# Kernel tuning notes

Hardware: AMD Instinct MI355X
Metric: run time of the kernel (lower is better)

The kernel has to match this reference:

```python
import jax, jax.numpy as jnp
import numpy as np

D_MODEL = 1024
NUM_HEADS = 16
D_K = D_MODEL // NUM_HEADS


def setup_inputs() -> dict:
    key = jax.random.key(0)
    k1, k2, k3, k4 = jax.random.split(key, 4)
    scale = 1.0 / np.sqrt(D_MODEL)
    inp = {
        "input": jax.random.normal(k1, (2, 2048, D_MODEL), dtype=jnp.float32),
        "W_qkv": jax.random.normal(k2, (D_MODEL, 3 * D_MODEL), dtype=jnp.float32) * scale,
        "b_qkv": jax.random.normal(k3, (3 * D_MODEL,), dtype=jnp.float32) * 0.02,
        "W_out": jax.random.normal(k4, (D_MODEL, D_MODEL), dtype=jnp.float32) * scale,
    }
    return inp


def reference(input, W_qkv, b_qkv, W_out):
    B, S, _ = input.shape
    qkv = input @ W_qkv + b_qkv                      # [B,S,3D]
    q, k, v = jnp.split(qkv, 3, axis=-1)             # each [B,S,D]
    def heads(x):
        return x.reshape(B, S, NUM_HEADS, D_K).transpose(0, 2, 1, 3)  # [B,H,S,dk]
    q, k, v = heads(q), heads(k), heads(v)
    scores = jnp.einsum("bhsd,bhtd->bhst", q, k) / jnp.sqrt(jnp.float32(D_K))
    attn = jax.nn.softmax(scores, axis=-1)           # [B,H,S,S]
    out = jnp.einsum("bhst,bhtd->bhsd", attn, v)     # [B,H,S,dk]
    out = out.transpose(0, 2, 1, 3).reshape(B, S, D_MODEL)
    return out @ W_out
```

## Files before the change

### kernel.cpp

```cpp
#include <hip/hip_runtime.h>

typedef unsigned short u16;
typedef unsigned int u32;
typedef __attribute__((ext_vector_type(8))) short short8;
typedef __attribute__((ext_vector_type(8))) __bf16 bf16x8;
typedef __attribute__((ext_vector_type(4))) float f32x4;
typedef __attribute__((ext_vector_type(16))) float f32x16;

__device__ __forceinline__ u16 f2bf(float f) {
  union { float f; u32 u; } c; c.f = f;
  u32 u = c.u + 0x7fffu + ((c.u >> 16) & 1u);
  return (u16)(u >> 16);
}
__device__ __forceinline__ f32x4 mfma16(short8 a, short8 b, f32x4 c) {
  return __builtin_amdgcn_mfma_f32_16x16x32_bf16(
      __builtin_bit_cast(bf16x8, a), __builtin_bit_cast(bf16x8, b), c, 0, 0, 0);
}
__device__ __forceinline__ f32x16 mfma32(short8 a, short8 b, f32x16 c) {
  return __builtin_amdgcn_mfma_f32_32x32x16_bf16(
      __builtin_bit_cast(bf16x8, a), __builtin_bit_cast(bf16x8, b), c, 0, 0, 0);
}
__device__ __forceinline__ float fexp2(float x) {
  float r; asm("v_exp_f32 %0, %1" : "=v"(r) : "v"(x)); return r;
}
__device__ __forceinline__ void gl16(const u16* g, u16* l) {
  __builtin_amdgcn_global_load_lds(
      (const __attribute__((address_space(1))) unsigned*)g,
      (__attribute__((address_space(3))) unsigned*)l, 16, 0, 0);
}

__global__ __launch_bounds__(256) void transpose_f32_bf16(const float* __restrict__ in,
                                                          u16* __restrict__ out,
                                                          int R, int C) {
  __shared__ u16 tile[32][33];
  int tx = threadIdx.x & 31, ty = threadIdx.x >> 5;
  int c0 = blockIdx.x * 32, r0 = blockIdx.y * 32;
  for (int i = 0; i < 32; i += 8)
    tile[ty + i][tx] = f2bf(in[(size_t)(r0 + ty + i) * C + c0 + tx]);
  __syncthreads();
  for (int i = 0; i < 32; i += 8)
    out[(size_t)(c0 + ty + i) * R + r0 + tx] = tile[tx][ty + i];
}

template <bool HAS_BIAS, bool AF32, bool OUTF32, bool ROUTE>
__global__ __launch_bounds__(256) void gemm_bt(const void* __restrict__ Av,
                                               const u16* __restrict__ BT,
                                               const float* __restrict__ bias,
                                               void* __restrict__ C0v,
                                               void* __restrict__ C1v,
                                               int M, int N, int K) {
  __shared__ __align__(16) u16 As[128 * 64];
  __shared__ __align__(16) u16 Bs[128 * 64];
  const int tid = threadIdx.x;
  const int w = tid >> 6, l = tid & 63;
  const int i16 = l & 15, q4 = l >> 4;

  const int nbx = gridDim.x;
  const int nwg = nbx * gridDim.y;
  int f = blockIdx.y * nbx + blockIdx.x;
  int wg = (nwg & 7) ? f : ((f & 7) * (nwg >> 3) + (f >> 3));
  const int m0 = (wg / nbx) * 128, n0 = (wg % nbx) * 128;
  const int wm = (w >> 1) * 64, wn = (w & 1) * 64;

  const int srow = l >> 3, skg = (l & 7) * 8;
  const int arow = tid >> 3, akg = (tid & 7) * 8;

  f32x4 acc[4][4] = {};
  float4 pf[4][2];
  if (AF32) {
#pragma unroll
    for (int i = 0; i < 4; ++i) {
      const float* src = (const float*)Av + (size_t)(m0 + arow + i * 32) * K + akg;
      pf[i][0] = *(const float4*)src;
      pf[i][1] = *(const float4*)(src + 4);
    }
  }

  for (int k0 = 0; k0 < K; k0 += 64) {
#pragma unroll
    for (int i = 0; i < 4; ++i) {
      const int seg = w * 4 + i, row = seg * 8 + srow;
      gl16(&BT[(size_t)(n0 + row) * K + k0 + skg], &Bs[seg * 512]);
    }
    if (AF32) {
#pragma unroll
      for (int i = 0; i < 4; ++i) {
        short8 v;
        v[0] = (short)f2bf(pf[i][0].x); v[1] = (short)f2bf(pf[i][0].y);
        v[2] = (short)f2bf(pf[i][0].z); v[3] = (short)f2bf(pf[i][0].w);
        v[4] = (short)f2bf(pf[i][1].x); v[5] = (short)f2bf(pf[i][1].y);
        v[6] = (short)f2bf(pf[i][1].z); v[7] = (short)f2bf(pf[i][1].w);
        *(short8*)&As[(arow + i * 32) * 64 + akg] = v;
      }
    } else {
#pragma unroll
      for (int i = 0; i < 4; ++i) {
        const int seg = w * 4 + i, row = seg * 8 + srow;
        gl16((const u16*)Av + (size_t)(m0 + row) * K + k0 + skg, &As[seg * 512]);
      }
    }
    __syncthreads();

    if (AF32 && k0 + 64 < K) {
#pragma unroll
      for (int i = 0; i < 4; ++i) {
        const float* src =
            (const float*)Av + (size_t)(m0 + arow + i * 32) * K + (k0 + 64) + akg;
        pf[i][0] = *(const float4*)src;
        pf[i][1] = *(const float4*)(src + 4);
      }
    }

#pragma unroll
    for (int ks = 0; ks < 2; ++ks) {
      short8 af[4], bfr[4];
#pragma unroll
      for (int mi = 0; mi < 4; ++mi)
        af[mi] = *(short8*)&As[(wm + mi * 16 + i16) * 64 + ks * 32 + q4 * 8];
#pragma unroll
      for (int ni = 0; ni < 4; ++ni)
        bfr[ni] = *(short8*)&Bs[(wn + ni * 16 + i16) * 64 + ks * 32 + q4 * 8];
#pragma unroll
      for (int mi = 0; mi < 4; ++mi)
#pragma unroll
        for (int ni = 0; ni < 4; ++ni)
          acc[mi][ni] = mfma16(af[mi], bfr[ni], acc[mi][ni]);
    }
    __syncthreads();
  }

  u16* dstb; float* dstf = nullptr; int ldc, cb;
  if (ROUTE) {
    if (n0 < 1024) { dstb = (u16*)C0v; ldc = 1024; cb = n0; }
    else           { dstb = (u16*)C1v; ldc = 2048; cb = n0 - 1024; }
  } else {
    if (OUTF32) dstf = (float*)C0v; else dstb = (u16*)C0v;
    ldc = N; cb = n0;
  }

  for (int mi = 0; mi < 4; ++mi) {
    int row = m0 + wm + mi * 16 + q4 * 4;
    for (int ni = 0; ni < 4; ++ni) {
      int nl = wn + ni * 16 + i16;
      float b = HAS_BIAS ? bias[n0 + nl] : 0.0f;
      for (int r = 0; r < 4; ++r) {
        float v = acc[mi][ni][r] + b;
        if (!ROUTE && OUTF32)
          dstf[(size_t)(row + r) * ldc + cb + nl] = v;
        else
          dstb[(size_t)(row + r) * ldc + cb + nl] = f2bf(v);
      }
    }
  }
}

__global__ __launch_bounds__(256) void attn_flash(u16* __restrict__ Qbuf,
                                                  const u16* __restrict__ KVall) {
  constexpr float CSC = 0.18033688011112042f;
  constexpr float MC  = 96.0f * CSC;
  __shared__ __align__(16) u16 Ks[2][64 * 72];
  __shared__ __align__(16) u16 Vt[2][64 * 72];
  __shared__ float RsumB[64], RsumT[64];

  const int tid = threadIdx.x;
  const int w = tid >> 6, l = tid & 63;
  const int l31 = l & 31, hi = l >> 5;
  const int qg = w >> 1, th = w & 1;

  const int L = blockIdx.x;
  const int xcd = L & 7, rr = L >> 3;
  const int qb = rr & 31, gg = rr >> 5;
  const int g = gg * 8 + xcd;
  const int h = g & 15, bat = g >> 4;
  const int q0 = qb * 64;

  u16* Q = Qbuf + (size_t)bat * 2048 * 1024;
  const u16* KV = KVall + (size_t)bat * 2048 * 2048;

  short8 qf[4];
  {
    const u16* qrow = Q + (size_t)(q0 + qg * 32 + l31) * 1024 + h * 64 + hi * 8;
#pragma unroll
    for (int ks = 0; ks < 4; ++ks) qf[ks] = *(const short8*)(qrow + ks * 16);
  }

  const int ht = qg * 64 + l;
  const int rb = ht >> 3;
  const int vc = ht & 7;
  const int cg = vc * 8;
  const u16* Kg = KV + h * 64 + cg;
  const u16* Vg = KV + 1024 + h * 64 + cg;
  u16* KsT = Ks[th];
  u16* VtT = Vt[th];
  const int tbase = th * 1024;

  short8 sk[4], sv[4];

#define LOADS(i_) {                                                          \
    const int t0_ = tbase + (i_) * 64;                                       \
    _Pragma("unroll") for (int ii = 0; ii < 4; ++ii)                         \
      sk[ii] = *(const short8*)&Kg[(size_t)(t0_ + rb + 16 * ii) * 2048];     \
    _Pragma("unroll") for (int ii = 0; ii < 2; ++ii) {                       \
      sv[2*ii]   = *(const short8*)&Vg[(size_t)(t0_ + 2*rb + 32*ii) * 2048]; \
      sv[2*ii+1] = *(const short8*)&Vg[(size_t)(t0_ + 2*rb + 32*ii + 1) * 2048]; } }

#define WRITES() {                                                           \
    _Pragma("unroll") for (int ii = 0; ii < 4; ++ii)                         \
      *(short8*)&KsT[(rb + 16 * ii) * 72 + cg] = sk[ii];                     \
    _Pragma("unroll") for (int ii = 0; ii < 2; ++ii) {                       \
      const int rho = rb + 16 * ii;                                          \
      _Pragma("unroll") for (int j = 0; j < 8; ++j) {                        \
        u32 wv = (u32)(u16)sv[2*ii][j] | ((u32)(u16)sv[2*ii+1][j] << 16);    \
        *(u32*)&VtT[(cg + j) * 72 + ((2 * rho) ^ (vc << 3))] = wv; } } }

  f32x16 o0 = {}, o1 = {};
  float sm0 = 0.f, sm1 = 0.f, sm2 = 0.f, sm3 = 0.f;

  const int sw0 = (l31 >> 3) << 3;
  const int sw1 = ((32 + l31) >> 3) << 3;

  LOADS(0);

  for (int i = 0; i < 16; ++i) {
    __syncthreads();
    WRITES();
    const int nx = (i + 1 < 16) ? i + 1 : 15;
    LOADS(nx);
    __syncthreads();

    f32x16 st0 = {}, st1 = {};
#pragma unroll
    for (int ks = 0; ks < 4; ++ks) {
      short8 kf0 = *(short8*)&KsT[l31 * 72 + ks * 16 + hi * 8];
      short8 kf1 = *(short8*)&KsT[(32 + l31) * 72 + ks * 16 + hi * 8];
      st0 = mfma32(kf0, qf[ks], st0);
      st1 = mfma32(kf1, qf[ks], st1);
    }

    u32 W[16];
#define SOFTMAX_PACK(stt, WB) {                                             \
      float p_[16];                                                         \
      _Pragma("unroll") for (int r = 0; r < 16; ++r)                        \
          p_[r] = fexp2(__builtin_fmaf(stt[r], CSC, -MC));                  \
      _Pragma("unroll") for (int r = 0; r < 16; r += 4) {                   \
        sm0 += p_[r]; sm1 += p_[r + 1]; sm2 += p_[r + 2]; sm3 += p_[r + 3]; \
      }                                                                     \
      _Pragma("unroll") for (int m = 0; m < 4; ++m)                         \
        _Pragma("unroll") for (int s = 0; s < 2; ++s)                       \
          asm("v_cvt_pk_bf16_f32 %0, %1, %2"                                \
              : "=v"(W[(WB) + m * 2 + s])                                   \
              : "v"(p_[4 * m + 2 * s]), "v"(p_[4 * m + 2 * s + 1]));        \
    }
    SOFTMAX_PACK(st0, 0)
    SOFTMAX_PACK(st1, 8)
#undef SOFTMAX_PACK

#pragma unroll
    for (int u = 0; u < 4; ++u) {
      const int base = (u >> 1) * 8 + (u & 1) * 4;
      u32 a0 = W[base], a1 = W[base + 1], b0 = W[base + 2], b1 = W[base + 3];
      asm("v_permlane32_swap_b32 %0, %1" : "+v"(a0), "+v"(b0));
      asm("v_permlane32_swap_b32 %0, %1" : "+v"(a1), "+v"(b1));
      int4 af4;
      af4.x = (int)a0; af4.y = (int)a1; af4.z = (int)b0; af4.w = (int)b1;
      const short8 pf = __builtin_bit_cast(short8, af4);
      const int toff = u * 16 + hi * 8;
      const short8 vf0 = *(short8*)&VtT[l31 * 72 + (toff ^ sw0)];
      const short8 vf1 = *(short8*)&VtT[(32 + l31) * 72 + (toff ^ sw1)];
      o0 = mfma32(pf, vf0, o0);
      o1 = mfma32(pf, vf1, o1);
    }
  }
#undef LOADS
#undef WRITES

  float rs = (sm0 + sm1) + (sm2 + sm3);
  rs += __shfl_xor(rs, 32);
  __syncthreads();
  float* MF = (float*)&Ks[0][0];
  if (th == 1) {
    float* dst = MF + (qg * 64 + l) * 36;
    *(f32x16*)dst = o0;
    *(f32x16*)(dst + 16) = o1;
    if (hi == 0) RsumB[qg * 32 + l31] = rs;
  }
  __syncthreads();
  float rtot = 0.f;
  if (th == 0) {
    const float* src = MF + (qg * 64 + l) * 36;
    o0 += *(const f32x16*)src;
    o1 += *(const f32x16*)(src + 16);
    rtot = rs + RsumB[qg * 32 + l31];
    if (hi == 0) RsumT[qg * 32 + l31] = rtot;
  }
  __syncthreads();
  if (th == 0) {
#pragma unroll
    for (int r = 0; r < 16; ++r) {
      const int qq = (r & 3) + 8 * (r >> 2) + 4 * hi;
      const float inv = 1.0f / RsumT[qg * 32 + qq];
      u16* dst = Q + (size_t)(q0 + qg * 32 + qq) * 1024 + h * 64 + l31;
      dst[0]  = f2bf(o0[r] * inv);
      dst[32] = f2bf(o1[r] * inv);
    }
  }
}

extern "C" void kernel_launch(void* const* d_in, const int* in_sizes, int n_in,
                              void* d_out, int out_size, void* d_ws, size_t ws_size,
                              hipStream_t stream) {
  const float* X    = (const float*)d_in[0];
  const float* Wqkv = (const float*)d_in[1];
  const float* bqkv = (const float*)d_in[2];
  const float* Wout = (const float*)d_in[3];

  u16* Qbuf = (u16*)d_out;
  u16* WT1  = Qbuf + (size_t)4096 * 1024;
  u16* WT2  = WT1 + (size_t)3072 * 1024;
  u16* KV   = (u16*)d_ws;
  float* Cws = (float*)d_ws;

  transpose_f32_bf16<<<dim3(96, 32), 256, 0, stream>>>(Wqkv, WT1, 1024, 3072);
  transpose_f32_bf16<<<dim3(32, 32), 256, 0, stream>>>(Wout, WT2, 1024, 1024);

  gemm_bt<true, true, false, true><<<dim3(24, 32), 256, 0, stream>>>(
      X, WT1, bqkv, Qbuf, KV, 4096, 3072, 1024);

  attn_flash<<<dim3(1024), 256, 0, stream>>>(Qbuf, KV);

  gemm_bt<false, false, true, false><<<dim3(8, 32), 256, 0, stream>>>(
      Qbuf, WT2, nullptr, Cws, nullptr, 4096, 1024, 1024);

  hipMemcpyAsync(d_out, Cws, (size_t)4096 * 1024 * sizeof(float),
                 hipMemcpyDeviceToDevice, stream);
}
```

Baseline: 232.6 us.

## Double-buffer GEMM LDS tiles and pre-convert input to bf16 when workspace allows

Gives the GEMM two LDS buffers for A and B, so loads for the next K tile are issued before the MFMA work on the current tile, and drops one barrier per iteration. When the workspace is large enough, the fp32 input is first converted to bf16 by a separate kernel, and the QKV GEMM then loads A asynchronously straight into LDS instead of converting it in registers. This doubles LDS use per block, which may lower occupancy, and adds an extra kernel launch plus extra memory traffic for the converted input.

```diff
diff --git a/kernel.cpp b/kernel.cpp
--- a/kernel.cpp
+++ b/kernel.cpp
@@ -42,6 +42,19 @@
     out[(size_t)(c0 + ty + i) * R + r0 + tx] = tile[tx][ty + i];
 }
 
+__global__ __launch_bounds__(256) void f32_to_bf16(const float* __restrict__ in,
+                                                   u16* __restrict__ out) {
+  const size_t base = ((size_t)blockIdx.x * 256 + threadIdx.x) * 8;
+  float4 f0 = *(const float4*)(in + base);
+  float4 f1 = *(const float4*)(in + base + 4);
+  short8 v;
+  v[0] = (short)f2bf(f0.x); v[1] = (short)f2bf(f0.y);
+  v[2] = (short)f2bf(f0.z); v[3] = (short)f2bf(f0.w);
+  v[4] = (short)f2bf(f1.x); v[5] = (short)f2bf(f1.y);
+  v[6] = (short)f2bf(f1.z); v[7] = (short)f2bf(f1.w);
+  *(short8*)&out[base] = v;
+}
+
 template <bool HAS_BIAS, bool AF32, bool OUTF32, bool ROUTE>
 __global__ __launch_bounds__(256) void gemm_bt(const void* __restrict__ Av,
                                                const u16* __restrict__ BT,
@@ -49,8 +62,8 @@
                                                void* __restrict__ C0v,
                                                void* __restrict__ C1v,
                                                int M, int N, int K) {
-  __shared__ __align__(16) u16 As[128 * 64];
-  __shared__ __align__(16) u16 Bs[128 * 64];
+  __shared__ __align__(16) u16 As[2][128 * 64];
+  __shared__ __align__(16) u16 Bs[2][128 * 64];
   const int tid = threadIdx.x;
   const int w = tid >> 6, l = tid & 63;
   const int i16 = l & 15, q4 = l >> 4;
@@ -67,59 +80,67 @@
 
   f32x4 acc[4][4] = {};
   float4 pf[4][2];
+
+#define STAGE_B(bufi, kk) {                                                  \
+    _Pragma("unroll") for (int i = 0; i < 4; ++i) {                          \
+      const int seg = w * 4 + i, row = seg * 8 + srow;                       \
+      gl16(&BT[(size_t)(n0 + row) * K + (kk) + skg], &Bs[bufi][seg * 512]); } }
+
+#define STAGE_A16(bufi, kk) {                                                \
+    _Pragma("unroll") for (int i = 0; i < 4; ++i) {                          \
+      const int seg = w * 4 + i, row = seg * 8 + srow;                       \
+      gl16((const u16*)Av + (size_t)(m0 + row) * K + (kk) + skg,             \
+           &As[bufi][seg * 512]); } }
+
+#define LOAD_PF(kk) {                                                        \
+    _Pragma("unroll") for (int i = 0; i < 4; ++i) {                          \
+      const float* src =                                                     \
+          (const float*)Av + (size_t)(m0 + arow + i * 32) * K + (kk) + akg;  \
+      pf[i][0] = *(const float4*)src;                                        \
+      pf[i][1] = *(const float4*)(src + 4); } }
+
+#define CVT_A(bufi) {                                                        \
+    _Pragma("unroll") for (int i = 0; i < 4; ++i) {                          \
+      short8 v;                                                              \
+      v[0] = (short)f2bf(pf[i][0].x); v[1] = (short)f2bf(pf[i][0].y);        \
+      v[2] = (short)f2bf(pf[i][0].z); v[3] = (short)f2bf(pf[i][0].w);        \
+      v[4] = (short)f2bf(pf[i][1].x); v[5] = (short)f2bf(pf[i][1].y);        \
+      v[6] = (short)f2bf(pf[i][1].z); v[7] = (short)f2bf(pf[i][1].w);        \
+      *(short8*)&As[bufi][(arow + i * 32) * 64 + akg] = v; } }
+
+  const int nk = K >> 6;
   if (AF32) {
-#pragma unroll
-    for (int i = 0; i < 4; ++i) {
-      const float* src = (const float*)Av + (size_t)(m0 + arow + i * 32) * K + akg;
-      pf[i][0] = *(const float4*)src;
-      pf[i][1] = *(const float4*)(src + 4);
-    }
-  }
-
-  for (int k0 = 0; k0 < K; k0 += 64) {
-#pragma unroll
-    for (int i = 0; i < 4; ++i) {
-      const int seg = w * 4 + i, row = seg * 8 + srow;
-      gl16(&BT[(size_t)(n0 + row) * K + k0 + skg], &Bs[seg * 512]);
-    }
-    if (AF32) {
-#pragma unroll
-      for (int i = 0; i < 4; ++i) {
-        short8 v;
-        v[0] = (short)f2bf(pf[i][0].x); v[1] = (short)f2bf(pf[i][0].y);
-        v[2] = (short)f2bf(pf[i][0].z); v[3] = (short)f2bf(pf[i][0].w);
-        v[4] = (short)f2bf(pf[i][1].x); v[5] = (short)f2bf(pf[i][1].y);
-        v[6] = (short)f2bf(pf[i][1].z); v[7] = (short)f2bf(pf[i][1].w);
-        *(short8*)&As[(arow + i * 32) * 64 + akg] = v;
+    LOAD_PF(0);
+    STAGE_B(0, 0);
+    CVT_A(0);
+    LOAD_PF(64);
+  } else {
+    STAGE_A16(0, 0);
+    STAGE_B(0, 0);
+  }
+  __syncthreads();
+
+  for (int t = 0; t < nk; ++t) {
+    const int cur = t & 1, nxt = cur ^ 1;
+    const int k1 = (t + 1) << 6;
+    if (t + 1 < nk) {
+      STAGE_B(nxt, k1);
+      if (AF32) {
+        CVT_A(nxt);
+        if (t + 2 < nk) LOAD_PF(k1 + 64);
+      } else {
+        STAGE_A16(nxt, k1);
       }
-    } else {
-#pragma unroll
-      for (int i = 0; i < 4; ++i) {
-        const int seg = w * 4 + i, row = seg * 8 + srow;
-        gl16((const u16*)Av + (size_t)(m0 + row) * K + k0 + skg, &As[seg * 512]);
-      }
-    }
-    __syncthreads();
-
-    if (AF32 && k0 + 64 < K) {
-#pragma unroll
-      for (int i = 0; i < 4; ++i) {
-        const float* src =
-            (const float*)Av + (size_t)(m0 + arow + i * 32) * K + (k0 + 64) + akg;
-        pf[i][0] = *(const float4*)src;
-        pf[i][1] = *(const float4*)(src + 4);
-      }
-    }
-
+    }
 #pragma unroll
     for (int ks = 0; ks < 2; ++ks) {
       short8 af[4], bfr[4];
 #pragma unroll
       for (int mi = 0; mi < 4; ++mi)
-        af[mi] = *(short8*)&As[(wm + mi * 16 + i16) * 64 + ks * 32 + q4 * 8];
+        af[mi] = *(short8*)&As[cur][(wm + mi * 16 + i16) * 64 + ks * 32 + q4 * 8];
 #pragma unroll
       for (int ni = 0; ni < 4; ++ni)
-        bfr[ni] = *(short8*)&Bs[(wn + ni * 16 + i16) * 64 + ks * 32 + q4 * 8];
+        bfr[ni] = *(short8*)&Bs[cur][(wn + ni * 16 + i16) * 64 + ks * 32 + q4 * 8];
 #pragma unroll
       for (int mi = 0; mi < 4; ++mi)
 #pragma unroll
@@ -128,6 +149,10 @@
     }
     __syncthreads();
   }
+#undef STAGE_B
+#undef STAGE_A16
+#undef LOAD_PF
+#undef CVT_A
 
   u16* dstb; float* dstf = nullptr; int ldc, cb;
   if (ROUTE) {
@@ -318,13 +343,22 @@
   u16* WT1  = Qbuf + (size_t)4096 * 1024;
   u16* WT2  = WT1 + (size_t)3072 * 1024;
   u16* KV   = (u16*)d_ws;
+  u16* Xbf  = KV + (size_t)4096 * 2048;
   float* Cws = (float*)d_ws;
+
+  const bool bigws = ws_size >= (size_t)24 * 1024 * 1024;
 
   transpose_f32_bf16<<<dim3(96, 32), 256, 0, stream>>>(Wqkv, WT1, 1024, 3072);
   transpose_f32_bf16<<<dim3(32, 32), 256, 0, stream>>>(Wout, WT2, 1024, 1024);
 
-  gemm_bt<true, true, false, true><<<dim3(24, 32), 256, 0, stream>>>(
-      X, WT1, bqkv, Qbuf, KV, 4096, 3072, 1024);
+  if (bigws) {
+    f32_to_bf16<<<dim3(2048), 256, 0, stream>>>(X, Xbf);
+    gemm_bt<true, false, false, true><<<dim3(24, 32), 256, 0, stream>>>(
+        Xbf, WT1, bqkv, Qbuf, KV, 4096, 3072, 1024);
+  } else {
+    gemm_bt<true, true, false, true><<<dim3(24, 32), 256, 0, stream>>>(
+        X, WT1, bqkv, Qbuf, KV, 4096, 3072, 1024);
+  }
 
   attn_flash<<<dim3(1024), 256, 0, stream>>>(Qbuf, KV);
 
```

New measurement: 228.8 us. About the same (-1.6%).

## Produce transposed V from GEMM, double-buffer GEMM and attention LDS via direct loads

Applied to the files above, without the earlier changes.

Splits the QKV projection into a Q/K GEMM and a separate GEMM that writes V already transposed, so attention can stage K and V^T tiles with direct global-to-LDS loads instead of register transposes. The GEMM gets a double-buffered LDS pipeline with an MFMA-fragment-ordered layout and padded rows for fp32-converted operands. Attention moves to 512-thread blocks covering 128 queries, with double-buffered K/V tiles and one barrier per iteration. The cost is an extra kernel launch and more LDS per block, which may limit occupancy.

```diff
diff --git a/kernel.cpp b/kernel.cpp
--- a/kernel.cpp
+++ b/kernel.cpp
@@ -42,84 +42,107 @@
     out[(size_t)(c0 + ty + i) * R + r0 + tx] = tile[tx][ty + i];
 }
 
-template <bool HAS_BIAS, bool AF32, bool OUTF32, bool ROUTE>
+template <int MODE>
 __global__ __launch_bounds__(256) void gemm_bt(const void* __restrict__ Av,
-                                               const u16* __restrict__ BT,
+                                               const void* __restrict__ Bv,
                                                const float* __restrict__ bias,
                                                void* __restrict__ C0v,
                                                void* __restrict__ C1v,
                                                int M, int N, int K) {
-  __shared__ __align__(16) u16 As[128 * 64];
-  __shared__ __align__(16) u16 Bs[128 * 64];
+  __shared__ __align__(16) u16 As[2][9216];
+  __shared__ __align__(16) u16 Bs[2][9216];
   const int tid = threadIdx.x;
   const int w = tid >> 6, l = tid & 63;
   const int i16 = l & 15, q4 = l >> 4;
 
   const int nbx = gridDim.x;
   const int nwg = nbx * gridDim.y;
-  int f = blockIdx.y * nbx + blockIdx.x;
-  int wg = (nwg & 7) ? f : ((f & 7) * (nwg >> 3) + (f >> 3));
+  int fid = blockIdx.y * nbx + blockIdx.x;
+  int wg = (nwg & 7) ? fid : ((fid & 7) * (nwg >> 3) + (fid >> 3));
   const int m0 = (wg / nbx) * 128, n0 = (wg % nbx) * 128;
   const int wm = (w >> 1) * 64, wn = (w & 1) * 64;
 
-  const int srow = l >> 3, skg = (l & 7) * 8;
   const int arow = tid >> 3, akg = (tid & 7) * 8;
+
+  const u16* A16p = (const u16*)Av;
+  const u16* B16p = (const u16*)Bv;
+  const float* Fp = (MODE == 1) ? (const float*)Av : (const float*)Bv;
+  const int fbase = (MODE == 1) ? m0 : n0;
 
   f32x4 acc[4][4] = {};
   float4 pf[4][2];
-  if (AF32) {
-#pragma unroll
-    for (int i = 0; i < 4; ++i) {
-      const float* src = (const float*)Av + (size_t)(m0 + arow + i * 32) * K + akg;
-      pf[i][0] = *(const float4*)src;
-      pf[i][1] = *(const float4*)(src + 4);
-    }
-  }
-
-  for (int k0 = 0; k0 < K; k0 += 64) {
-#pragma unroll
-    for (int i = 0; i < 4; ++i) {
-      const int seg = w * 4 + i, row = seg * 8 + srow;
-      gl16(&BT[(size_t)(n0 + row) * K + k0 + skg], &Bs[seg * 512]);
-    }
-    if (AF32) {
-#pragma unroll
-      for (int i = 0; i < 4; ++i) {
-        short8 v;
-        v[0] = (short)f2bf(pf[i][0].x); v[1] = (short)f2bf(pf[i][0].y);
-        v[2] = (short)f2bf(pf[i][0].z); v[3] = (short)f2bf(pf[i][0].w);
-        v[4] = (short)f2bf(pf[i][1].x); v[5] = (short)f2bf(pf[i][1].y);
-        v[6] = (short)f2bf(pf[i][1].z); v[7] = (short)f2bf(pf[i][1].w);
-        *(short8*)&As[(arow + i * 32) * 64 + akg] = v;
-      }
-    } else {
-#pragma unroll
-      for (int i = 0; i < 4; ++i) {
-        const int seg = w * 4 + i, row = seg * 8 + srow;
-        gl16((const u16*)Av + (size_t)(m0 + row) * K + k0 + skg, &As[seg * 512]);
-      }
-    }
-    __syncthreads();
-
-    if (AF32 && k0 + 64 < K) {
-#pragma unroll
-      for (int i = 0; i < 4; ++i) {
-        const float* src =
-            (const float*)Av + (size_t)(m0 + arow + i * 32) * K + (k0 + 64) + akg;
-        pf[i][0] = *(const float4*)src;
-        pf[i][1] = *(const float4*)(src + 4);
-      }
-    }
-
+
+#define STAGE_A16(bufi, kk) {                                                  \
+    _Pragma("unroll") for (int i = 0; i < 4; ++i) {                            \
+      const int s = w * 4 + i;                                                 \
+      gl16(&A16p[(size_t)(m0 + (s >> 1) * 16 + i16) * K + (kk) + (s & 1) * 32  \
+                 + q4 * 8],                                                    \
+           &As[bufi][s * 512]); } }
+#define STAGE_B16(bufi, kk) {                                                  \
+    _Pragma("unroll") for (int i = 0; i < 4; ++i) {                            \
+      const int s = w * 4 + i;                                                 \
+      gl16(&B16p[(size_t)(n0 + (s >> 1) * 16 + i16) * K + (kk) + (s & 1) * 32  \
+                 + q4 * 8],                                                    \
+           &Bs[bufi][s * 512]); } }
+#define LOAD_PFX(kk) {                                                         \
+    _Pragma("unroll") for (int i = 0; i < 4; ++i) {                            \
+      const float* src = Fp + (size_t)(fbase + arow + i * 32) * K + (kk) + akg;\
+      pf[i][0] = *(const float4*)src;                                          \
+      pf[i][1] = *(const float4*)(src + 4); } }
+#define CVT_X(bufi) {                                                          \
+    _Pragma("unroll") for (int i = 0; i < 4; ++i) {                            \
+      short8 v;                                                                \
+      v[0] = (short)f2bf(pf[i][0].x); v[1] = (short)f2bf(pf[i][0].y);          \
+      v[2] = (short)f2bf(pf[i][0].z); v[3] = (short)f2bf(pf[i][0].w);          \
+      v[4] = (short)f2bf(pf[i][1].x); v[5] = (short)f2bf(pf[i][1].y);          \
+      v[6] = (short)f2bf(pf[i][1].z); v[7] = (short)f2bf(pf[i][1].w);          \
+      u16* d = (MODE == 1) ? &As[bufi][(arow + i * 32) * 72 + akg]             \
+                           : &Bs[bufi][(arow + i * 32) * 72 + akg];            \
+      *(short8*)d = v; } }
+
+  const int nk = K >> 6;
+  if constexpr (MODE == 0) {
+    STAGE_A16(0, 0); STAGE_B16(0, 0);
+  } else if constexpr (MODE == 1) {
+    LOAD_PFX(0); STAGE_B16(0, 0); CVT_X(0); LOAD_PFX(64);
+  } else {
+    LOAD_PFX(0); STAGE_A16(0, 0); CVT_X(0); LOAD_PFX(64);
+  }
+  __syncthreads();
+
+  for (int t = 0; t < nk; ++t) {
+    const int cur = t & 1, nxt = cur ^ 1;
+    const int k1 = (t + 1) << 6;
+    if (t + 1 < nk) {
+      if constexpr (MODE == 0) {
+        STAGE_A16(nxt, k1); STAGE_B16(nxt, k1);
+      } else if constexpr (MODE == 1) {
+        STAGE_B16(nxt, k1); CVT_X(nxt);
+        if (t + 2 < nk) LOAD_PFX(k1 + 64);
+      } else {
+        STAGE_A16(nxt, k1); CVT_X(nxt);
+        if (t + 2 < nk) LOAD_PFX(k1 + 64);
+      }
+    }
 #pragma unroll
     for (int ks = 0; ks < 2; ++ks) {
       short8 af[4], bfr[4];
 #pragma unroll
-      for (int mi = 0; mi < 4; ++mi)
-        af[mi] = *(short8*)&As[(wm + mi * 16 + i16) * 64 + ks * 32 + q4 * 8];
-#pragma unroll
-      for (int ni = 0; ni < 4; ++ni)
-        bfr[ni] = *(short8*)&Bs[(wn + ni * 16 + i16) * 64 + ks * 32 + q4 * 8];
+      for (int mi = 0; mi < 4; ++mi) {
+        if constexpr (MODE == 1)
+          af[mi] = *(short8*)&As[cur][(wm + mi * 16 + i16) * 72 + ks * 32 + q4 * 8];
+        else
+          af[mi] = *(short8*)((char*)&As[cur][0] +
+                              (((wm >> 4) + mi) * 2 + ks) * 1024 + l * 16);
+      }
+#pragma unroll
+      for (int ni = 0; ni < 4; ++ni) {
+        if constexpr (MODE == 2)
+          bfr[ni] = *(short8*)&Bs[cur][(wn + ni * 16 + i16) * 72 + ks * 32 + q4 * 8];
+        else
+          bfr[ni] = *(short8*)((char*)&Bs[cur][0] +
+                               (((wn >> 4) + ni) * 2 + ks) * 1024 + l * 16);
+      }
 #pragma unroll
       for (int mi = 0; mi < 4; ++mi)
 #pragma unroll
@@ -128,54 +151,76 @@
     }
     __syncthreads();
   }
-
-  u16* dstb; float* dstf = nullptr; int ldc, cb;
-  if (ROUTE) {
-    if (n0 < 1024) { dstb = (u16*)C0v; ldc = 1024; cb = n0; }
-    else           { dstb = (u16*)C1v; ldc = 2048; cb = n0 - 1024; }
+#undef STAGE_A16
+#undef STAGE_B16
+#undef LOAD_PFX
+#undef CVT_X
+
+  if constexpr (MODE == 0) {
+    float* dstf = (float*)C0v;
+    for (int mi = 0; mi < 4; ++mi) {
+      int row = m0 + wm + mi * 16 + q4 * 4;
+      for (int ni = 0; ni < 4; ++ni) {
+        int nl = wn + ni * 16 + i16;
+        for (int r = 0; r < 4; ++r)
+          dstf[(size_t)(row + r) * N + n0 + nl] = acc[mi][ni][r];
+      }
+    }
+  } else if constexpr (MODE == 1) {
+    u16* dstb; int cb;
+    if (n0 < 1024) { dstb = (u16*)C0v; cb = n0; }
+    else           { dstb = (u16*)C1v; cb = n0 - 1024; }
+    for (int mi = 0; mi < 4; ++mi) {
+      int row = m0 + wm + mi * 16 + q4 * 4;
+      for (int ni = 0; ni < 4; ++ni) {
+        int nl = wn + ni * 16 + i16;
+        float b = bias[n0 + nl];
+        for (int r = 0; r < 4; ++r)
+          dstb[(size_t)(row + r) * 1024 + cb + nl] = f2bf(acc[mi][ni][r] + b);
+      }
+    }
   } else {
-    if (OUTF32) dstf = (float*)C0v; else dstb = (u16*)C0v;
-    ldc = N; cb = n0;
-  }
-
-  for (int mi = 0; mi < 4; ++mi) {
-    int row = m0 + wm + mi * 16 + q4 * 4;
-    for (int ni = 0; ni < 4; ++ni) {
-      int nl = wn + ni * 16 + i16;
-      float b = HAS_BIAS ? bias[n0 + nl] : 0.0f;
-      for (int r = 0; r < 4; ++r) {
-        float v = acc[mi][ni][r] + b;
-        if (!ROUTE && OUTF32)
-          dstf[(size_t)(row + r) * ldc + cb + nl] = v;
-        else
-          dstb[(size_t)(row + r) * ldc + cb + nl] = f2bf(v);
-      }
-    }
-  }
-}
-
-__global__ __launch_bounds__(256) void attn_flash(u16* __restrict__ Qbuf,
-                                                  const u16* __restrict__ KVall) {
+    u16* dstb = (u16*)C0v + ((n0 >= 2048) ? (size_t)1024 * 2048 : 0);
+    const int cb = n0 & 2047;
+    for (int mi = 0; mi < 4; ++mi) {
+      int row = m0 + wm + mi * 16 + q4 * 4;
+      float4 bv = *(const float4*)&bias[row];
+      const float bvr[4] = {bv.x, bv.y, bv.z, bv.w};
+      for (int ni = 0; ni < 4; ++ni) {
+        int nl = wn + ni * 16 + i16;
+        for (int r = 0; r < 4; ++r)
+          dstb[(size_t)(row + r) * 2048 + cb + nl] = f2bf(acc[mi][ni][r] + bvr[r]);
+      }
+    }
+  }
+}
+
+__global__ __launch_bounds__(512, 4) void attn_flash(u16* __restrict__ Qbuf,
+                                                     const u16* __restrict__ Kall,
+                                                     const u16* __restrict__ VTall) {
   constexpr float CSC = 0.18033688011112042f;
   constexpr float MC  = 96.0f * CSC;
-  __shared__ __align__(16) u16 Ks[2][64 * 72];
-  __shared__ __align__(16) u16 Vt[2][64 * 72];
-  __shared__ float RsumB[64], RsumT[64];
+  __shared__ __align__(16) u16 SH[32768];
+  __shared__ float RsumB[128], RsumT[128];
 
   const int tid = threadIdx.x;
   const int w = tid >> 6, l = tid & 63;
   const int l31 = l & 31, hi = l >> 5;
   const int qg = w >> 1, th = w & 1;
 
+  u16* KsL = SH + th * 16384;
+  u16* VsL = SH + th * 16384 + 8192;
+
   const int L = blockIdx.x;
   const int xcd = L & 7, rr = L >> 3;
-  const int qb = rr & 31, gg = rr >> 5;
+  const int qb = rr & 15, gg = rr >> 4;
   const int g = gg * 8 + xcd;
   const int h = g & 15, bat = g >> 4;
-  const int q0 = qb * 64;
+  const int q0 = qb * 128;
 
   u16* Q = Qbuf + (size_t)bat * 2048 * 1024;
-  const u16* KV = KVall + (size_t)bat * 2048 * 2048;
+  const u16* Kb = Kall + (size_t)bat * 2048 * 1024;
+  const u16* Vtb = VTall + (size_t)bat * 1024 * 2048;
 
   short8 qf[4];
   {
@@ -184,55 +229,37 @@
     for (int ks = 0; ks < 4; ++ks) qf[ks] = *(const short8*)(qrow + ks * 16);
   }
 
-  const int ht = qg * 64 + l;
-  const int rb = ht >> 3;
-  const int vc = ht & 7;
-  const int cg = vc * 8;
-  const u16* Kg = KV + h * 64 + cg;
-  const u16* Vg = KV + 1024 + h * 64 + cg;
-  u16* KsT = Ks[th];
-  u16* VtT = Vt[th];
+  const u16* Ksrc = Kb + (size_t)((qg & 1) * 32 + l31) * 1024 + h * 64 +
+                    (qg >> 1) * 16 + hi * 8;
+  const u16* Vsrc = Vtb + (size_t)(h * 64 + (qg & 1) * 32 + l31) * 2048 +
+                    (qg >> 1) * 16 + hi * 8;
   const int tbase = th * 1024;
 
-  short8 sk[4], sv[4];
-
-#define LOADS(i_) {                                                          \
-    const int t0_ = tbase + (i_) * 64;                                       \
-    _Pragma("unroll") for (int ii = 0; ii < 4; ++ii)                         \
-      sk[ii] = *(const short8*)&Kg[(size_t)(t0_ + rb + 16 * ii) * 2048];     \
-    _Pragma("unroll") for (int ii = 0; ii < 2; ++ii) {                       \
-      sv[2*ii]   = *(const short8*)&Vg[(size_t)(t0_ + 2*rb + 32*ii) * 2048]; \
-      sv[2*ii+1] = *(const short8*)&Vg[(size_t)(t0_ + 2*rb + 32*ii + 1) * 2048]; } }
-
-#define WRITES() {                                                           \
-    _Pragma("unroll") for (int ii = 0; ii < 4; ++ii)                         \
-      *(short8*)&KsT[(rb + 16 * ii) * 72 + cg] = sk[ii];                     \
-    _Pragma("unroll") for (int ii = 0; ii < 2; ++ii) {                       \
-      const int rho = rb + 16 * ii;                                          \
-      _Pragma("unroll") for (int j = 0; j < 8; ++j) {                        \
-        u32 wv = (u32)(u16)sv[2*ii][j] | ((u32)(u16)sv[2*ii+1][j] << 16);    \
-        *(u32*)&VtT[(cg + j) * 72 + ((2 * rho) ^ (vc << 3))] = wv; } } }
+#define STAGE(buf_, t0_) {                                                   \
+    const size_t tk = (size_t)(t0_) * 1024;                                  \
+    gl16(Ksrc + tk,      KsL + (buf_) * 4096 + qg * 512);                    \
+    gl16(Ksrc + tk + 32, KsL + (buf_) * 4096 + (qg + 4) * 512);              \
+    gl16(Vsrc + (t0_),      VsL + (buf_) * 4096 + qg * 512);                 \
+    gl16(Vsrc + (t0_) + 32, VsL + (buf_) * 4096 + (qg + 4) * 512); }
 
   f32x16 o0 = {}, o1 = {};
   float sm0 = 0.f, sm1 = 0.f, sm2 = 0.f, sm3 = 0.f;
 
-  const int sw0 = (l31 >> 3) << 3;
-  const int sw1 = ((32 + l31) >> 3) << 3;
-
-  LOADS(0);
+  STAGE(0, tbase);
+  __syncthreads();
 
   for (int i = 0; i < 16; ++i) {
-    __syncthreads();
-    WRITES();
-    const int nx = (i + 1 < 16) ? i + 1 : 15;
-    LOADS(nx);
-    __syncthreads();
+    const int cur = i & 1;
+    if (i + 1 < 16) STAGE(cur ^ 1, tbase + (i + 1) * 64);
+
+    const char* Kc = (const char*)KsL + cur * 8192 + l * 16;
+    const char* Vc = (const char*)VsL + cur * 8192 + l * 16;
 
     f32x16 st0 = {}, st1 = {};
 #pragma unroll
     for (int ks = 0; ks < 4; ++ks) {
-      short8 kf0 = *(short8*)&KsT[l31 * 72 + ks * 16 + hi * 8];
-      short8 kf1 = *(short8*)&KsT[(32 + l31) * 72 + ks * 16 + hi * 8];
+      short8 kf0 = *(const short8*)(Kc + ks * 2048);
+      short8 kf1 = *(const short8*)(Kc + ks * 2048 + 1024);
       st0 = mfma32(kf0, qf[ks], st0);
       st1 = mfma32(kf1, qf[ks], st1);
     }
@@ -263,21 +290,20 @@
       asm("v_permlane32_swap_b32 %0, %1" : "+v"(a1), "+v"(b1));
       int4 af4;
       af4.x = (int)a0; af4.y = (int)a1; af4.z = (int)b0; af4.w = (int)b1;
-      const short8 pf = __builtin_bit_cast(short8, af4);
-      const int toff = u * 16 + hi * 8;
-      const short8 vf0 = *(short8*)&VtT[l31 * 72 + (toff ^ sw0)];
-      const short8 vf1 = *(short8*)&VtT[(32 + l31) * 72 + (toff ^ sw1)];
-      o0 = mfma32(pf, vf0, o0);
-      o1 = mfma32(pf, vf1, o1);
-    }
-  }
-#undef LOADS
-#undef WRITES
+      const short8 pfr = __builtin_bit_cast(short8, af4);
+      const short8 vf0 = *(const short8*)(Vc + u * 2048);
+      const short8 vf1 = *(const short8*)(Vc + u * 2048 + 1024);
+      o0 = mfma32(pfr, vf0, o0);
+      o1 = mfma32(pfr, vf1, o1);
+    }
+    __syncthreads();
+  }
+#undef STAGE
 
   float rs = (sm0 + sm1) + (sm2 + sm3);
   rs += __shfl_xor(rs, 32);
   __syncthreads();
-  float* MF = (float*)&Ks[0][0];
+  float* MF = (float*)SH;
   if (th == 1) {
     float* dst = MF + (qg * 64 + l) * 36;
     *(f32x16*)dst = o0;
@@ -285,12 +311,11 @@
     if (hi == 0) RsumB[qg * 32 + l31] = rs;
   }
   __syncthreads();
-  float rtot = 0.f;
   if (th == 0) {
     const float* src = MF + (qg * 64 + l) * 36;
     o0 += *(const f32x16*)src;
     o1 += *(const f32x16*)(src + 16);
-    rtot = rs + RsumB[qg * 32 + l31];
+    float rtot = rs + RsumB[qg * 32 + l31];
     if (hi == 0) RsumT[qg * 32 + l31] = rtot;
   }
   __syncthreads();
@@ -317,18 +342,22 @@
   u16* Qbuf = (u16*)d_out;
   u16* WT1  = Qbuf + (size_t)4096 * 1024;
   u16* WT2  = WT1 + (size_t)3072 * 1024;
-  u16* KV   = (u16*)d_ws;
+  u16* Kbuf = (u16*)d_ws;
+  u16* VT   = Kbuf + (size_t)4096 * 1024;
   float* Cws = (float*)d_ws;
 
   transpose_f32_bf16<<<dim3(96, 32), 256, 0, stream>>>(Wqkv, WT1, 1024, 3072);
   transpose_f32_bf16<<<dim3(32, 32), 256, 0, stream>>>(Wout, WT2, 1024, 1024);
 
-  gemm_bt<true, true, false, true><<<dim3(24, 32), 256, 0, stream>>>(
-      X, WT1, bqkv, Qbuf, KV, 4096, 3072, 1024);
-
-  attn_flash<<<dim3(1024), 256, 0, stream>>>(Qbuf, KV);
-
-  gemm_bt<false, false, true, false><<<dim3(8, 32), 256, 0, stream>>>(
+  gemm_bt<1><<<dim3(16, 32), 256, 0, stream>>>(
+      X, WT1, bqkv, Qbuf, Kbuf, 4096, 2048, 1024);
+
+  gemm_bt<2><<<dim3(32, 8), 256, 0, stream>>>(
+      WT1 + (size_t)2048 * 1024, X, bqkv + 2048, VT, nullptr, 1024, 4096, 1024);
+
+  attn_flash<<<dim3(512), 512, 0, stream>>>(Qbuf, Kbuf, VT);
+
+  gemm_bt<0><<<dim3(8, 32), 256, 0, stream>>>(
       Qbuf, WT2, nullptr, Cws, nullptr, 4096, 1024, 1024);
 
   hipMemcpyAsync(d_out, Cws, (size_t)4096 * 1024 * sizeof(float),
```

After: 228.0 us. 1.02x faster.
